# Optimization experiments

Measured on AMD Instinct MI355X. Metric: run time of the kernel, lower is better.

## Reference

```python
import jax, jax.numpy as jnp
import numpy as np

N_NODES = 50000


def gcn_conv(x, src, dst, W, b, deg_inv_sqrt):
    # PyG GCNConv: add self-loops, symmetric normalization D^-1/2 A D^-1/2,
    # linear transform, scatter-add aggregation, bias.
    xw = x @ W  # [N, F_out]
    norm = deg_inv_sqrt[src] * deg_inv_sqrt[dst]  # [E]
    agg = jax.ops.segment_sum(norm[:, None] * xw[src], dst, num_segments=N_NODES)
    # self-loop contribution: norm_ii = deg_i^-1
    agg = agg + xw * (deg_inv_sqrt * deg_inv_sqrt)[:, None]
    return agg + b


def setup_inputs() -> dict:
    key = jax.random.key(0)
    ks = jax.random.split(key, 6)
    N, E, F_in, F_out = N_NODES, 800000, 128, 64
    x = jax.random.normal(ks[0], (N, F_in), dtype=jnp.float32)
    edge_index = jax.random.randint(ks[1], (2, E), 0, N, dtype=jnp.int64)
    scale1 = 1.0 / np.sqrt(F_in)
    scale2 = 1.0 / np.sqrt(2 * F_out)
    W1 = jax.random.normal(ks[2], (F_in, 2 * F_out), dtype=jnp.float32) * scale1
    b1 = jnp.zeros((2 * F_out,), dtype=jnp.float32)
    W_mu = jax.random.normal(ks[3], (2 * F_out, F_out), dtype=jnp.float32) * scale2
    b_mu = jnp.zeros((F_out,), dtype=jnp.float32)
    W_ls = jax.random.normal(ks[4], (2 * F_out, F_out), dtype=jnp.float32) * scale2
    b_ls = jnp.zeros((F_out,), dtype=jnp.float32)
    return {"x": x, "edge_index": edge_index, "W1": W1, "b1": b1,
            "W_mu": W_mu, "b_mu": b_mu, "W_ls": W_ls, "b_ls": b_ls}


def reference(x, edge_index, W1, b1, W_mu, b_mu, W_ls, b_ls):
    src, dst = edge_index[0], edge_index[1]
    # degree (incl. self-loop) on destination nodes
    deg = jax.ops.segment_sum(jnp.ones_like(dst, dtype=x.dtype), dst,
                              num_segments=N_NODES) + 1.0
    deg_inv_sqrt = jax.lax.rsqrt(deg)
    h = jax.nn.relu(gcn_conv(x, src, dst, W1, b1, deg_inv_sqrt))
    # dropout in eval mode -> identity (deterministic reference)
    mu = gcn_conv(h, src, dst, W_mu, b_mu, deg_inv_sqrt)
    logstd = gcn_conv(h, src, dst, W_ls, b_ls, deg_inv_sqrt)
    return mu, logstd
```

## Files before the change

kernel.cpp:

```cpp
#include <hip/hip_runtime.h>
#include <hip/hip_fp16.h>

#define N_NODES 50000
#define CAP 64
#define UNR 16

__global__ void k_scatter(const int* __restrict__ idx, int E,
                          int* __restrict__ cursor, int* __restrict__ esrc) {
    int e = blockIdx.x * blockDim.x + threadIdx.x;
    if (e >= E) return;
    int s = idx[e], d = idx[E + e];
    int pos = atomicAdd(&cursor[d], 1);
    if (pos < CAP) esrc[(size_t)d * CAP + pos] = s;
}

__global__ void k_rsqrt(const int* __restrict__ deg, float* __restrict__ dis, int n) {
    int i = blockIdx.x * blockDim.x + threadIdx.x;
    if (i < n) dis[i] = rsqrtf((float)deg[i] + 1.0f);
}

__global__ void k_wcat(const float* __restrict__ wmu, const float* __restrict__ wls,
                       float* __restrict__ wcat) {
    int i = blockIdx.x * blockDim.x + threadIdx.x;
    if (i >= 128 * 128) return;
    int k = i >> 7, j = i & 127;
    wcat[i] = (j < 64) ? wmu[k * 64 + j] : wls[k * 64 + (j - 64)];
}

template <bool IN_HALF>
__global__ __launch_bounds__(256) void k_gemm(const void* __restrict__ Ain,
                                              const float* __restrict__ W,
                                              const float* __restrict__ rowscale,
                                              __half* __restrict__ C, int nrows) {
    __shared__ float Ws[32][128];
    __shared__ float Xs[64][32];
    int t = threadIdx.x;
    int tx = t & 31;
    int ty = t >> 5;
    int row0 = blockIdx.x * 64;
    float acc[8][4] = {};

    for (int kb = 0; kb < 4; ++kb) {
        const float4* wsrc = (const float4*)(W + (size_t)kb * 32 * 128);
        float4* wdst = (float4*)(&Ws[0][0]);
        for (int i = t; i < 1024; i += 256) wdst[i] = wsrc[i];

        if constexpr (!IN_HALF) {
            const float* Af = (const float*)Ain;
            for (int j = t; j < 512; j += 256) {
                int r = j >> 3, c4 = j & 7;
                int row = row0 + r;
                float4 v = make_float4(0.f, 0.f, 0.f, 0.f);
                if (row < nrows)
                    v = *(const float4*)(Af + (size_t)row * 128 + kb * 32 + c4 * 4);
                *(float4*)(&Xs[r][c4 * 4]) = v;
            }
        } else {
            const __half* Ah = (const __half*)Ain;
            int r = t >> 2, c8 = (t & 3) * 8;
            int row = row0 + r;
            union { float4 f; __half2 h[4]; } u;
            u.f = make_float4(0.f, 0.f, 0.f, 0.f);
            if (row < nrows)
                u.f = *(const float4*)(Ah + (size_t)row * 128 + kb * 32 + c8);
            float* xp = &Xs[r][c8];
            #pragma unroll
            for (int q = 0; q < 4; ++q) {
                float2 f2 = __half22float2(u.h[q]);
                xp[q * 2] = f2.x;
                xp[q * 2 + 1] = f2.y;
            }
        }
        __syncthreads();

        #pragma unroll
        for (int kq = 0; kq < 8; ++kq) {
            float4 xv[8];
            #pragma unroll
            for (int r = 0; r < 8; ++r)
                xv[r] = *(const float4*)(&Xs[ty * 8 + r][kq * 4]);
            #pragma unroll
            for (int kk = 0; kk < 4; ++kk) {
                float4 w = *(const float4*)(&Ws[kq * 4 + kk][tx * 4]);
                #pragma unroll
                for (int r = 0; r < 8; ++r) {
                    float xs = (kk == 0) ? xv[r].x : (kk == 1) ? xv[r].y
                             : (kk == 2) ? xv[r].z : xv[r].w;
                    acc[r][0] = fmaf(xs, w.x, acc[r][0]);
                    acc[r][1] = fmaf(xs, w.y, acc[r][1]);
                    acc[r][2] = fmaf(xs, w.z, acc[r][2]);
                    acc[r][3] = fmaf(xs, w.w, acc[r][3]);
                }
            }
        }
        __syncthreads();
    }

    #pragma unroll
    for (int r = 0; r < 8; ++r) {
        int row = row0 + ty * 8 + r;
        if (row < nrows) {
            float s = rowscale[row];
            union { float2 f; __half2 h[2]; } o;
            o.h[0] = __float22half2_rn(make_float2(acc[r][0] * s, acc[r][1] * s));
            o.h[1] = __float22half2_rn(make_float2(acc[r][2] * s, acc[r][3] * s));
            *(float2*)(C + (size_t)row * 128 + tx * 4) = o.f;
        }
    }
}

__global__ __launch_bounds__(256) void k_agg1(const int* __restrict__ deg,
                                              const int* __restrict__ esrc,
                                              const __half* __restrict__ xw,
                                              const float* __restrict__ dis,
                                              const float* __restrict__ b1,
                                              __half* __restrict__ h, int n) {
    int d = blockIdx.x * 4 + (threadIdx.x >> 6);
    int lane = threadIdx.x & 63;
    if (d >= n) return;
    const int* bucket = esrc + (size_t)d * CAP;
    int cnt = min(deg[d], CAP);
    float ax = 0.f, ay = 0.f;
    for (int e = 0; e < cnt; e += UNR) {
        int sj[UNR]; bool okj[UNR];
        #pragma unroll
        for (int j = 0; j < UNR; ++j) {
            int ee = e + j;
            okj[j] = ee < cnt;
            sj[j] = bucket[okj[j] ? ee : 0];
        }
        __half2 v[UNR];
        #pragma unroll
        for (int j = 0; j < UNR; ++j)
            v[j] = *(const __half2*)(xw + (size_t)sj[j] * 128 + lane * 2);
        #pragma unroll
        for (int j = 0; j < UNR; ++j) {
            float2 f = __half22float2(v[j]);
            ax += okj[j] ? f.x : 0.f;
            ay += okj[j] ? f.y : 0.f;
        }
    }
    float ds = dis[d];
    float2 sv = __half22float2(*(const __half2*)(xw + (size_t)d * 128 + lane * 2));
    float2 bb = *(const float2*)(b1 + lane * 2);
    float rx = fmaxf(fmaf(ds, ax + sv.x, bb.x), 0.f);
    float ry = fmaxf(fmaf(ds, ay + sv.y, bb.y), 0.f);
    *(__half2*)(h + (size_t)d * 128 + lane * 2) = __float22half2_rn(make_float2(rx, ry));
}

__global__ __launch_bounds__(256) void k_agg2(const int* __restrict__ deg,
                                              const int* __restrict__ esrc,
                                              const __half* __restrict__ hw,
                                              const float* __restrict__ dis,
                                              const float* __restrict__ bmu,
                                              const float* __restrict__ bls,
                                              float* __restrict__ out, int n) {
    int d = blockIdx.x * 4 + (threadIdx.x >> 6);
    int lane = threadIdx.x & 63;
    if (d >= n) return;
    const int* bucket = esrc + (size_t)d * CAP;
    int cnt = min(deg[d], CAP);
    float ax = 0.f, ay = 0.f;
    for (int e = 0; e < cnt; e += UNR) {
        int sj[UNR]; bool okj[UNR];
        #pragma unroll
        for (int j = 0; j < UNR; ++j) {
            int ee = e + j;
            okj[j] = ee < cnt;
            sj[j] = bucket[okj[j] ? ee : 0];
        }
        __half2 v[UNR];
        #pragma unroll
        for (int j = 0; j < UNR; ++j)
            v[j] = *(const __half2*)(hw + (size_t)sj[j] * 128 + lane * 2);
        #pragma unroll
        for (int j = 0; j < UNR; ++j) {
            float2 f = __half22float2(v[j]);
            ax += okj[j] ? f.x : 0.f;
            ay += okj[j] ? f.y : 0.f;
        }
    }
    float ds = dis[d];
    float2 sv = __half22float2(*(const __half2*)(hw + (size_t)d * 128 + lane * 2));
    float2 bb = (lane < 32) ? *(const float2*)(bmu + lane * 2)
                            : *(const float2*)(bls + (lane - 32) * 2);
    float rx = fmaf(ds, ax + sv.x, bb.x);
    float ry = fmaf(ds, ay + sv.y, bb.y);
    float* op = (lane < 32) ? out + (size_t)d * 64 + lane * 2
                            : out + (size_t)N_NODES * 64 + (size_t)d * 64 + (lane - 32) * 2;
    *(float2*)op = make_float2(rx, ry);
}

extern "C" void kernel_launch(void* const* d_in, const int* in_sizes, int n_in,
                              void* d_out, int out_size, void* d_ws, size_t ws_size,
                              hipStream_t stream) {
    const float* x   = (const float*)d_in[0];
    const int*   idx = (const int*)d_in[1];
    const float* W1  = (const float*)d_in[2];
    const float* b1  = (const float*)d_in[3];
    const float* Wmu = (const float*)d_in[4];
    const float* bmu = (const float*)d_in[5];
    const float* Wls = (const float*)d_in[6];
    const float* bls = (const float*)d_in[7];
    int E = in_sizes[1] / 2;
    float* out = (float*)d_out;

    char* ws = (char*)d_ws;
    size_t off = 0;
    auto alloc = [&](size_t bytes) { void* p = ws + off; off += (bytes + 15) & ~15ull; return p; };
    int*    cursor = (int*)alloc(N_NODES * 4);
    float*  dis    = (float*)alloc(N_NODES * 4);
    float*  wcat   = (float*)alloc(16384 * 4);
    int*    esrc   = (int*)alloc((size_t)N_NODES * CAP * 4);
    __half* A16    = (__half*)alloc((size_t)N_NODES * 128 * 2);
    __half* B16    = (__half*)alloc((size_t)N_NODES * 128 * 2);
    __half* C16    = A16;

    hipMemsetAsync(cursor, 0, N_NODES * sizeof(int), stream);
    k_scatter<<<(E + 255) / 256, 256, 0, stream>>>(idx, E, cursor, esrc);
    k_rsqrt<<<(N_NODES + 255) / 256, 256, 0, stream>>>(cursor, dis, N_NODES);

    k_gemm<false><<<(N_NODES + 63) / 64, 256, 0, stream>>>(x, W1, dis, A16, N_NODES);
    k_agg1<<<(N_NODES + 3) / 4, 256, 0, stream>>>(cursor, esrc, A16, dis, b1, B16, N_NODES);

    k_wcat<<<(16384 + 255) / 256, 256, 0, stream>>>(Wmu, Wls, wcat);
    k_gemm<true><<<(N_NODES + 63) / 64, 256, 0, stream>>>(B16, wcat, dis, C16, N_NODES);
    k_agg2<<<(N_NODES + 3) / 4, 256, 0, stream>>>(cursor, esrc, C16, dis, bmu, bls, out, N_NODES);
}
```

Before: 257.2 us.

## Rewrite node-feature GEMM with fp16 MFMA instructions

Replaces the scalar FP32 tiled GEMM with a kernel that stages the whole 128-wide input tile and a transposed fp16 copy of W in shared memory, then computes with 16x16x32 fp16 MFMA intrinsics per wavefront. This cuts the ALU cost of the two dense transforms. In exchange, inputs and weights are rounded to fp16, every block re-transposes the full weight matrix, and the output is written as scalar half stores instead of vector stores. Workspace alignment is also raised to 64 bytes.

```diff
diff --git a/kernel.cpp b/kernel.cpp
--- a/kernel.cpp
+++ b/kernel.cpp
@@ -4,6 +4,9 @@
 #define N_NODES 50000
 #define CAP 64
 #define UNR 16
+
+typedef __attribute__((ext_vector_type(8))) _Float16 half8;
+typedef __attribute__((ext_vector_type(4))) float f32x4;
 
 __global__ void k_scatter(const int* __restrict__ idx, int E,
                           int* __restrict__ cursor, int* __restrict__ esrc) {
@@ -32,79 +35,75 @@
                                               const float* __restrict__ W,
                                               const float* __restrict__ rowscale,
                                               __half* __restrict__ C, int nrows) {
-    __shared__ float Ws[32][128];
-    __shared__ float Xs[64][32];
+    __shared__ _Float16 As[64][136];
+    __shared__ _Float16 Wt[128][136];
     int t = threadIdx.x;
-    int tx = t & 31;
-    int ty = t >> 5;
     int row0 = blockIdx.x * 64;
-    float acc[8][4] = {};
-
-    for (int kb = 0; kb < 4; ++kb) {
-        const float4* wsrc = (const float4*)(W + (size_t)kb * 32 * 128);
-        float4* wdst = (float4*)(&Ws[0][0]);
-        for (int i = t; i < 1024; i += 256) wdst[i] = wsrc[i];
-
-        if constexpr (!IN_HALF) {
-            const float* Af = (const float*)Ain;
-            for (int j = t; j < 512; j += 256) {
-                int r = j >> 3, c4 = j & 7;
-                int row = row0 + r;
-                float4 v = make_float4(0.f, 0.f, 0.f, 0.f);
-                if (row < nrows)
-                    v = *(const float4*)(Af + (size_t)row * 128 + kb * 32 + c4 * 4);
-                *(float4*)(&Xs[r][c4 * 4]) = v;
-            }
-        } else {
-            const __half* Ah = (const __half*)Ain;
-            int r = t >> 2, c8 = (t & 3) * 8;
+
+    for (int i = t; i < 16384; i += 256) {
+        int k = i >> 7, n = i & 127;
+        Wt[n][k] = (_Float16)W[i];
+    }
+    if constexpr (!IN_HALF) {
+        const float* Af = (const float*)Ain;
+        for (int i = t; i < 2048; i += 256) {
+            int r = i >> 5, c4 = i & 31;
             int row = row0 + r;
-            union { float4 f; __half2 h[4]; } u;
-            u.f = make_float4(0.f, 0.f, 0.f, 0.f);
+            float4 v = make_float4(0.f, 0.f, 0.f, 0.f);
+            if (row < nrows) v = *(const float4*)(Af + (size_t)row * 128 + c4 * 4);
+            _Float16* dst = &As[r][c4 * 4];
+            dst[0] = (_Float16)v.x; dst[1] = (_Float16)v.y;
+            dst[2] = (_Float16)v.z; dst[3] = (_Float16)v.w;
+        }
+    } else {
+        const __half* Ah = (const __half*)Ain;
+        for (int i = t; i < 1024; i += 256) {
+            int r = i >> 4, c8 = i & 15;
+            int row = row0 + r;
+            half8 v = {};
+            if (row < nrows) v = *(const half8*)(Ah + (size_t)row * 128 + c8 * 8);
+            *(half8*)&As[r][c8 * 8] = v;
+        }
+    }
+    __syncthreads();
+
+    int wid = t >> 6, lane = t & 63;
+    int l15 = lane & 15, kg = lane >> 4;
+    int koff = kg * 8;
+
+    half8 a[4];
+    int arow = wid * 16 + l15;
+    #pragma unroll
+    for (int kc = 0; kc < 4; ++kc)
+        a[kc] = *(const half8*)&As[arow][kc * 32 + koff];
+
+    f32x4 acc[8];
+    #pragma unroll
+    for (int nt = 0; nt < 8; ++nt) acc[nt] = (f32x4){0.f, 0.f, 0.f, 0.f};
+
+    #pragma unroll
+    for (int nt = 0; nt < 8; ++nt) {
+        int bcol = nt * 16 + l15;
+        #pragma unroll
+        for (int kc = 0; kc < 4; ++kc) {
+            half8 b = *(const half8*)&Wt[bcol][kc * 32 + koff];
+            acc[nt] = __builtin_amdgcn_mfma_f32_16x16x32_f16(a[kc], b, acc[nt], 0, 0, 0);
+        }
+    }
+
+    int rbase = row0 + wid * 16 + kg * 4;
+    float rs[4];
+    #pragma unroll
+    for (int r = 0; r < 4; ++r)
+        rs[r] = (rbase + r < nrows) ? rowscale[rbase + r] : 1.0f;
+    #pragma unroll
+    for (int nt = 0; nt < 8; ++nt) {
+        int col = nt * 16 + l15;
+        #pragma unroll
+        for (int r = 0; r < 4; ++r) {
+            int row = rbase + r;
             if (row < nrows)
-                u.f = *(const float4*)(Ah + (size_t)row * 128 + kb * 32 + c8);
-            float* xp = &Xs[r][c8];
-            #pragma unroll
-            for (int q = 0; q < 4; ++q) {
-                float2 f2 = __half22float2(u.h[q]);
-                xp[q * 2] = f2.x;
-                xp[q * 2 + 1] = f2.y;
-            }
-        }
-        __syncthreads();
-
-        #pragma unroll
-        for (int kq = 0; kq < 8; ++kq) {
-            float4 xv[8];
-            #pragma unroll
-            for (int r = 0; r < 8; ++r)
-                xv[r] = *(const float4*)(&Xs[ty * 8 + r][kq * 4]);
-            #pragma unroll
-            for (int kk = 0; kk < 4; ++kk) {
-                float4 w = *(const float4*)(&Ws[kq * 4 + kk][tx * 4]);
-                #pragma unroll
-                for (int r = 0; r < 8; ++r) {
-                    float xs = (kk == 0) ? xv[r].x : (kk == 1) ? xv[r].y
-                             : (kk == 2) ? xv[r].z : xv[r].w;
-                    acc[r][0] = fmaf(xs, w.x, acc[r][0]);
-                    acc[r][1] = fmaf(xs, w.y, acc[r][1]);
-                    acc[r][2] = fmaf(xs, w.z, acc[r][2]);
-                    acc[r][3] = fmaf(xs, w.w, acc[r][3]);
-                }
-            }
-        }
-        __syncthreads();
-    }
-
-    #pragma unroll
-    for (int r = 0; r < 8; ++r) {
-        int row = row0 + ty * 8 + r;
-        if (row < nrows) {
-            float s = rowscale[row];
-            union { float2 f; __half2 h[2]; } o;
-            o.h[0] = __float22half2_rn(make_float2(acc[r][0] * s, acc[r][1] * s));
-            o.h[1] = __float22half2_rn(make_float2(acc[r][2] * s, acc[r][3] * s));
-            *(float2*)(C + (size_t)row * 128 + tx * 4) = o.f;
+                C[(size_t)row * 128 + col] = __float2half(acc[nt][r] * rs[r]);
         }
     }
 }
@@ -207,7 +206,7 @@
 
     char* ws = (char*)d_ws;
     size_t off = 0;
-    auto alloc = [&](size_t bytes) { void* p = ws + off; off += (bytes + 15) & ~15ull; return p; };
+    auto alloc = [&](size_t bytes) { void* p = ws + off; off += (bytes + 63) & ~63ull; return p; };
     int*    cursor = (int*)alloc(N_NODES * 4);
     float*  dis    = (float*)alloc(N_NODES * 4);
     float*  wcat   = (float*)alloc(16384 * 4);
```

Result: faster. 243.8 us (-5.2%).
